# Kernel optimization log

Measured on AMD Instinct MI355X. Metric: run time of the kernel, lower is better.

The kernel has to match this reference:

```python
import jax, jax.numpy as jnp
import numpy as np

N = 131072   # n_nodes == n_edges (required by the broadcast in the original module)
C = 256      # node_channels == edge_channels (required by the broadcast)
EPS_BN = 1e-5
EPS = 1e-5


def _linear_params(key, out_c, in_c):
    k1, k2 = jax.random.split(key)
    bound = 1.0 / np.sqrt(in_c)
    W = jax.random.uniform(k1, (out_c, in_c), minval=-bound, maxval=bound, dtype=jnp.float32)
    b = jax.random.uniform(k2, (out_c,), minval=-bound, maxval=bound, dtype=jnp.float32)
    return W, b


def setup_inputs() -> dict:
    key = jax.random.key(0)
    ks = jax.random.split(key, 10)
    h = jax.random.normal(ks[0], (N, C), dtype=jnp.float32)
    e = jax.random.normal(ks[1], (N, C), dtype=jnp.float32)
    edge_index = jax.random.randint(ks[2], (2, N), 0, N, dtype=jnp.int64)
    A_w, A_b = _linear_params(ks[3], C, C)
    B_w, B_b = _linear_params(ks[4], C, C)
    C_w, C_b = _linear_params(ks[5], C, C)
    D_w, D_b = _linear_params(ks[6], C, C)
    U_w, U_b = _linear_params(ks[7], C, C)
    V_w, V_b = _linear_params(ks[8], C, C)
    bn_gamma = jnp.ones((C,), dtype=jnp.float32)
    bn_beta = jnp.zeros((C,), dtype=jnp.float32)
    return dict(h=h, edge_index=edge_index, e=e,
                A_w=A_w, A_b=A_b, B_w=B_w, B_b=B_b,
                C_w=C_w, C_b=C_b, D_w=D_w, D_b=D_b,
                bn_gamma=bn_gamma, bn_beta=bn_beta,
                U_w=U_w, U_b=U_b, V_w=V_w, V_b=V_b)


def reference(h, edge_index, e,
              A_w, A_b, B_w, B_b, C_w, C_b, D_w, D_b,
              bn_gamma, bn_beta, U_w, U_b, V_w, V_b):
    row, col = edge_index[0], edge_index[1]
    # gather + four parallel linears, summed: [E, C]
    e_out = (h[row] @ A_w.T + A_b
             + h[col] @ B_w.T + B_b
             + e[col] @ C_w.T + C_b
             + e[row] @ D_w.T + D_b)
    # BatchNorm1d (training mode: batch stats, biased variance) + ReLU
    mu = jnp.mean(e_out, axis=0)
    var = jnp.var(e_out, axis=0)
    e_out = jax.nn.relu(bn_gamma * (e_out - mu) * jax.lax.rsqrt(var + EPS_BN) + bn_beta)
    # scatter-add edge messages into node-indexed e, then sigmoid-normalize over dim 0
    e_new = e.at[row].add(e_out)
    e_new = jax.nn.sigmoid(e_new)
    e_new = e_new / (jnp.sum(e_new, axis=0, keepdims=True) + EPS)
    # final gather-multiply-reduce: (e_new * V(h[col])).sum(0) broadcasts [N,C]*[E,C] with N==E
    h_out = h @ U_w.T + U_b + jnp.sum(e_new * (h[col] @ V_w.T + V_b), axis=0)
    h_out = jax.nn.relu(h_out)
    return h_out, e_new
```

## Files before the change

### kernel.cpp

```cpp
#include <hip/hip_runtime.h>
#include <hip/hip_bf16.h>


typedef __attribute__((ext_vector_type(8))) short bf16x8;
typedef __attribute__((ext_vector_type(4))) float f32x4;

__device__ __forceinline__ float b2f(unsigned int lo16) {
  union { unsigned int u; float f; } c; c.u = lo16 << 16; return c.f;
}
__device__ __forceinline__ float lof(unsigned int u) { return b2f(u & 0xffffu); }
__device__ __forceinline__ float hif(unsigned int u) { return b2f(u >> 16); }
__device__ __forceinline__ unsigned int f2b(float f) {
  union { float f; unsigned int u; } c; c.f = f;
  unsigned int u = c.u;
  u += 0x7fffu + ((u >> 16) & 1u);
  return u >> 16;
}

__global__ __launch_bounds__(256) void prep_tiled(const float* __restrict__ src,
                                                  unsigned short* __restrict__ dst,
                                                  int nChunks) {
  int g = blockIdx.x * 256 + threadIdx.x;
  if (g >= nChunks) return;
  int mtile = g >> 9;
  int rem = g & 511;
  int r = rem >> 5, k8 = rem & 31;
  const float4* s = reinterpret_cast<const float4*>(src + (((size_t)mtile * 16 + r) << 8) + k8 * 8);
  float4 v0 = s[0], v1 = s[1];
  uint4 o;
  o.x = f2b(v0.x) | (f2b(v0.y) << 16);
  o.y = f2b(v0.z) | (f2b(v0.w) << 16);
  o.z = f2b(v1.x) | (f2b(v1.y) << 16);
  o.w = f2b(v1.z) | (f2b(v1.w) << 16);
  *reinterpret_cast<uint4*>(dst + ((size_t)mtile * 512 + k8 * 16 + r) * 8) = o;
}

__global__ __launch_bounds__(256) void gemm_bt(const unsigned short* __restrict__ At,
                                               const unsigned short* __restrict__ Bt,
                                               const float* __restrict__ bias,
                                               unsigned short* __restrict__ Cmat,
                                               int O, int nColBlk) {
  __shared__ char lds[16384];
  const int bid = blockIdx.x;
  const int colBlk = bid % nColBlk;
  const int rowBlk = bid / nColBlk;
  const int tid = threadIdx.x;
  const int w = tid >> 6, lane = tid & 63;
  const int wm = w >> 1, wn = w & 1;

  const char* Abase = (const char*)At + (size_t)(rowBlk * 8 + w * 2) * 8192 + lane * 16;
  const char* Bbase = (const char*)Bt + (size_t)(colBlk * 8 + w * 2) * 8192 + lane * 16;
  char* ldsA0 = lds + (w * 2) * 1024;
  char* ldsA1 = lds + (w * 2 + 1) * 1024;
  char* ldsB0 = lds + 8192 + (w * 2) * 1024;
  char* ldsB1 = lds + 8192 + (w * 2 + 1) * 1024;

  f32x4 acc[4][4] = {};

  for (int kt = 0; kt < 8; ++kt) {
    const size_t ko = (size_t)kt * 1024;
    __builtin_amdgcn_global_load_lds((const __attribute__((address_space(1))) void*)(Abase + ko),
                                     (__attribute__((address_space(3))) void*)ldsA0, 16, 0, 0);
    __builtin_amdgcn_global_load_lds((const __attribute__((address_space(1))) void*)(Abase + 8192 + ko),
                                     (__attribute__((address_space(3))) void*)ldsA1, 16, 0, 0);
    __builtin_amdgcn_global_load_lds((const __attribute__((address_space(1))) void*)(Bbase + ko),
                                     (__attribute__((address_space(3))) void*)ldsB0, 16, 0, 0);
    __builtin_amdgcn_global_load_lds((const __attribute__((address_space(1))) void*)(Bbase + 8192 + ko),
                                     (__attribute__((address_space(3))) void*)ldsB1, 16, 0, 0);
    __syncthreads();
    bf16x8 a[4], b[4];
#pragma unroll
    for (int mi = 0; mi < 4; ++mi)
      a[mi] = *reinterpret_cast<const bf16x8*>(lds + (wm * 4 + mi) * 1024 + lane * 16);
#pragma unroll
    for (int ni = 0; ni < 4; ++ni)
      b[ni] = *reinterpret_cast<const bf16x8*>(lds + 8192 + (wn * 4 + ni) * 1024 + lane * 16);
#pragma unroll
    for (int mi = 0; mi < 4; ++mi)
#pragma unroll
      for (int ni = 0; ni < 4; ++ni)
        acc[mi][ni] = __builtin_amdgcn_mfma_f32_16x16x32_bf16(a[mi], b[ni], acc[mi][ni], 0, 0, 0);
    __syncthreads();
  }

  const int rb = rowBlk * 128 + wm * 64 + ((lane >> 4) << 2);
  const int cb = colBlk * 128 + wn * 64 + (lane & 15);
#pragma unroll
  for (int mi = 0; mi < 4; ++mi) {
#pragma unroll
    for (int ni = 0; ni < 4; ++ni) {
      const int coln = cb + ni * 16;
      const float bz = bias[coln];
      const size_t base = (size_t)(rb + mi * 16) * O + coln;
#pragma unroll
      for (int r = 0; r < 4; ++r)
        Cmat[base + (size_t)r * O] = (unsigned short)f2b(acc[mi][ni][r] + bz);
    }
  }
}

__global__ __launch_bounds__(256) void edge_sum(
    const unsigned short* __restrict__ Ph, const unsigned short* __restrict__ Pe,
    const int* __restrict__ ei, const int* __restrict__ modep,
    unsigned short* __restrict__ eout,
    float* __restrict__ sums, float* __restrict__ sumsq, int Nn) {
  __shared__ float red[8][256];
  const int c8 = threadIdx.x & 31;
  const int sub = threadIdx.x >> 5;
  const int mode = *modep;
  float s[8], q[8];
#pragma unroll
  for (int j = 0; j < 8; ++j) { s[j] = 0.f; q[j] = 0.f; }

#pragma unroll 1
  for (int it = 0; it < 8; ++it) {
    const int k = blockIdx.x * 64 + it * 8 + sub;
    int row, col;
    if (mode) { row = ei[2 * k]; col = ei[2 * (Nn + k)]; }
    else      { row = ei[k];     col = ei[Nn + k]; }
    const uint4 ha = *reinterpret_cast<const uint4*>(Ph + (size_t)row * 1024 + c8 * 8);
    const uint4 hb = *reinterpret_cast<const uint4*>(Ph + (size_t)col * 1024 + 256 + c8 * 8);
    const uint4 ec = *reinterpret_cast<const uint4*>(Pe + (size_t)col * 512 + c8 * 8);
    const uint4 ed = *reinterpret_cast<const uint4*>(Pe + (size_t)row * 512 + 256 + c8 * 8);
    const unsigned int aw[4] = {ha.x, ha.y, ha.z, ha.w};
    const unsigned int bw[4] = {hb.x, hb.y, hb.z, hb.w};
    const unsigned int cw[4] = {ec.x, ec.y, ec.z, ec.w};
    const unsigned int dw[4] = {ed.x, ed.y, ed.z, ed.w};
    unsigned int ow[4];
#pragma unroll
    for (int p = 0; p < 4; ++p) {
      float v0 = lof(aw[p]) + lof(bw[p]) + lof(cw[p]) + lof(dw[p]);
      float v1 = hif(aw[p]) + hif(bw[p]) + hif(cw[p]) + hif(dw[p]);
      s[2 * p] += v0;     q[2 * p] += v0 * v0;
      s[2 * p + 1] += v1; q[2 * p + 1] += v1 * v1;
      ow[p] = f2b(v0) | (f2b(v1) << 16);
    }
    uint4 o; o.x = ow[0]; o.y = ow[1]; o.z = ow[2]; o.w = ow[3];
    *reinterpret_cast<uint4*>(eout + (size_t)k * 256 + c8 * 8) = o;
  }
#pragma unroll
  for (int j = 0; j < 8; ++j) red[sub][c8 * 8 + j] = s[j];
  __syncthreads();
  {
    const int c = threadIdx.x;
    float t = 0.f;
#pragma unroll
    for (int u2 = 0; u2 < 8; ++u2) t += red[u2][c];
    atomicAdd(sums + c, t);
  }
  __syncthreads();
#pragma unroll
  for (int j = 0; j < 8; ++j) red[sub][c8 * 8 + j] = q[j];
  __syncthreads();
  {
    const int c = threadIdx.x;
    float t = 0.f;
#pragma unroll
    for (int u2 = 0; u2 < 8; ++u2) t += red[u2][c];
    atomicAdd(sumsq + c, t);
  }
}

__global__ void bn_finalize(const float* __restrict__ sums, const float* __restrict__ sumsq,
                            const float* __restrict__ gamma, const float* __restrict__ beta,
                            float* __restrict__ scale, float* __restrict__ shift, float invE) {
  const int c = threadIdx.x;
  const float mu = sums[c] * invE;
  const float var = fmaxf(sumsq[c] * invE - mu * mu, 0.f);
  const float sc = gamma[c] * rsqrtf(var + 1e-5f);
  scale[c] = sc;
  shift[c] = beta[c] - mu * sc;
}

__global__ __launch_bounds__(256) void hist_rows(const int* __restrict__ ei,
                                                 const int* __restrict__ modep,
                                                 int* __restrict__ cnt, int Nn) {
  const int k = blockIdx.x * 256 + threadIdx.x;
  if (k >= Nn) return;
  const int row = (*modep) ? ei[2 * k] : ei[k];
  atomicAdd(&cnt[row], 1);
}

__global__ __launch_bounds__(256) void scan1(const int* __restrict__ cnt,
                                             int* __restrict__ bsum) {
  __shared__ int red[256];
  const int t = threadIdx.x;
  red[t] = cnt[blockIdx.x * 256 + t];
  __syncthreads();
#pragma unroll
  for (int s = 128; s > 0; s >>= 1) {
    if (t < s) red[t] += red[t + s];
    __syncthreads();
  }
  if (t == 0) bsum[blockIdx.x] = red[0];
}

__global__ __launch_bounds__(512) void scan2(int* __restrict__ bsum, int nb) {
  __shared__ int tmp[512];
  const int t = threadIdx.x;
  const int own = (t < nb) ? bsum[t] : 0;
  tmp[t] = own;
  __syncthreads();
  for (int off = 1; off < 512; off <<= 1) {
    int v = (t >= off) ? tmp[t - off] : 0;
    __syncthreads();
    tmp[t] += v;
    __syncthreads();
  }
  if (t < nb) bsum[t] = tmp[t] - own;
}

__global__ __launch_bounds__(256) void scan3(const int* __restrict__ cnt,
                                             const int* __restrict__ bsum,
                                             int* __restrict__ base, int Nn) {
  __shared__ int tmp[256];
  const int t = threadIdx.x;
  const int gid = blockIdx.x * 256 + t;
  const int own = cnt[gid];
  tmp[t] = own;
  __syncthreads();
  for (int off = 1; off < 256; off <<= 1) {
    int v = (t >= off) ? tmp[t - off] : 0;
    __syncthreads();
    tmp[t] += v;
    __syncthreads();
  }
  base[gid] = tmp[t] - own + bsum[blockIdx.x];
  if (gid == 0) base[Nn] = Nn;
}

__global__ __launch_bounds__(256) void scatter_eids(const int* __restrict__ ei,
                                                    const int* __restrict__ modep,
                                                    const int* __restrict__ base,
                                                    int* __restrict__ cnt,
                                                    int* __restrict__ sorted, int Nn) {
  const int k = blockIdx.x * 256 + threadIdx.x;
  if (k >= Nn) return;
  const int row = (*modep) ? ei[2 * k] : ei[k];
  const int pos = base[row] + atomicAdd(&cnt[row], -1) - 1;
  sorted[pos] = k;
}

__global__ __launch_bounds__(256) void gather_sig_colsum(
    const float* __restrict__ e, const unsigned short* __restrict__ eout,
    const int* __restrict__ base, const int* __restrict__ sorted,
    const float* __restrict__ scale, const float* __restrict__ shift,
    float* __restrict__ acc, float* __restrict__ colsum) {
  __shared__ float red[4][256];
  const int lane = threadIdx.x & 63, w = threadIdx.x >> 6;
  const float4 sc = *reinterpret_cast<const float4*>(scale + lane * 4);
  const float4 sh = *reinterpret_cast<const float4*>(shift + lane * 4);
  float s0 = 0.f, s1 = 0.f, s2 = 0.f, s3 = 0.f;
  const int n0 = blockIdx.x * 64 + w * 16;
#pragma unroll 1
  for (int it = 0; it < 16; ++it) {
    const int i = n0 + it;
    float4 v = *reinterpret_cast<const float4*>(e + (size_t)i * 256 + lane * 4);
    const int p0 = base[i], p1 = base[i + 1];
#pragma unroll 1
    for (int p = p0; p < p1; ++p) {
      const int eid = sorted[p];
      const uint2 wv = *reinterpret_cast<const uint2*>(eout + (size_t)eid * 256 + lane * 4);
      v.x += fmaxf(fmaf(sc.x, lof(wv.x), sh.x), 0.f);
      v.y += fmaxf(fmaf(sc.y, hif(wv.x), sh.y), 0.f);
      v.z += fmaxf(fmaf(sc.z, lof(wv.y), sh.z), 0.f);
      v.w += fmaxf(fmaf(sc.w, hif(wv.y), sh.w), 0.f);
    }
    v.x = 1.f / (1.f + __expf(-v.x));
    v.y = 1.f / (1.f + __expf(-v.y));
    v.z = 1.f / (1.f + __expf(-v.z));
    v.w = 1.f / (1.f + __expf(-v.w));
    *reinterpret_cast<float4*>(acc + (size_t)i * 256 + lane * 4) = v;
    s0 += v.x; s1 += v.y; s2 += v.z; s3 += v.w;
  }
  red[w][lane * 4 + 0] = s0;
  red[w][lane * 4 + 1] = s1;
  red[w][lane * 4 + 2] = s2;
  red[w][lane * 4 + 3] = s3;
  __syncthreads();
  const int c = threadIdx.x;
  atomicAdd(colsum + c, red[0][c] + red[1][c] + red[2][c] + red[3][c]);
}

__global__ void inv_finalize(const float* __restrict__ colsum, float* __restrict__ inv) {
  const int c = threadIdx.x;
  inv[c] = 1.0f / (colsum[c] + 1e-5f);
}

__global__ __launch_bounds__(256) void enew_T(
    const float* __restrict__ acc, const float* __restrict__ inv,
    const int* __restrict__ ei, const int* __restrict__ modep,
    const unsigned short* __restrict__ Ph,
    float* __restrict__ outE, float* __restrict__ T, int Nn) {
  __shared__ float red[8][256];
  const int c8 = threadIdx.x & 31, sub = threadIdx.x >> 5;
  const int mode = *modep;
  float iv[8];
#pragma unroll
  for (int j = 0; j < 8; ++j) iv[j] = inv[c8 * 8 + j];
  float t[8];
#pragma unroll
  for (int j = 0; j < 8; ++j) t[j] = 0.f;
#pragma unroll 1
  for (int it = 0; it < 8; ++it) {
    const int k = blockIdx.x * 64 + it * 8 + sub;
    const int col = mode ? ei[2 * (Nn + k)] : ei[Nn + k];
    const float4* p0 = reinterpret_cast<const float4*>(acc + (size_t)k * 256 + c8 * 8);
    const float4 a = p0[0], b = p0[1];
    float en[8] = {a.x * iv[0], a.y * iv[1], a.z * iv[2], a.w * iv[3],
                   b.x * iv[4], b.y * iv[5], b.z * iv[6], b.w * iv[7]};
    float4 o0, o1;
    o0.x = en[0]; o0.y = en[1]; o0.z = en[2]; o0.w = en[3];
    o1.x = en[4]; o1.y = en[5]; o1.z = en[6]; o1.w = en[7];
    float4* q0 = reinterpret_cast<float4*>(outE + (size_t)k * 256 + c8 * 8);
    q0[0] = o0; q0[1] = o1;
    const uint4 hv = *reinterpret_cast<const uint4*>(Ph + (size_t)col * 1024 + 512 + c8 * 8);
    const unsigned int w4[4] = {hv.x, hv.y, hv.z, hv.w};
#pragma unroll
    for (int p = 0; p < 4; ++p) {
      t[2 * p] += en[2 * p] * lof(w4[p]);
      t[2 * p + 1] += en[2 * p + 1] * hif(w4[p]);
    }
  }
#pragma unroll
  for (int j = 0; j < 8; ++j) red[sub][c8 * 8 + j] = t[j];
  __syncthreads();
  {
    const int c = threadIdx.x;
    float tt = 0.f;
#pragma unroll
    for (int u2 = 0; u2 < 8; ++u2) tt += red[u2][c];
    atomicAdd(T + c, tt);
  }
}

__global__ __launch_bounds__(256) void hout_k(
    const unsigned short* __restrict__ Ph, const float* __restrict__ T,
    float* __restrict__ outH, int nChunks) {
  const int g = blockIdx.x * 256 + threadIdx.x;
  if (g >= nChunks) return;
  const int i = g >> 5, c8 = g & 31;
  const uint4 hu = *reinterpret_cast<const uint4*>(Ph + (size_t)i * 1024 + 768 + c8 * 8);
  const float4 t0 = *reinterpret_cast<const float4*>(T + c8 * 8);
  const float4 t1 = *reinterpret_cast<const float4*>(T + c8 * 8 + 4);
  float4 o0, o1;
  o0.x = fmaxf(lof(hu.x) + t0.x, 0.f);
  o0.y = fmaxf(hif(hu.x) + t0.y, 0.f);
  o0.z = fmaxf(lof(hu.y) + t0.z, 0.f);
  o0.w = fmaxf(hif(hu.y) + t0.w, 0.f);
  o1.x = fmaxf(lof(hu.z) + t1.x, 0.f);
  o1.y = fmaxf(hif(hu.z) + t1.y, 0.f);
  o1.z = fmaxf(lof(hu.w) + t1.z, 0.f);
  o1.w = fmaxf(hif(hu.w) + t1.w, 0.f);
  float4* q = reinterpret_cast<float4*>(outH + (size_t)i * 256 + c8 * 8);
  q[0] = o0; q[1] = o1;
}

__global__ void pack_bias(const float* a, const float* b, const float* v, const float* u,
                          const float* cc, const float* dd,
                          float* biasH, float* biasE) {
  const int t = threadIdx.x;
  biasH[t] = a[t]; biasH[256 + t] = b[t]; biasH[512 + t] = v[t]; biasH[768 + t] = u[t];
  biasE[t] = cc[t]; biasE[256 + t] = dd[t];
}

__global__ void detect_idx(const int* __restrict__ ei, int* __restrict__ mode) {
  if (threadIdx.x == 0 && blockIdx.x == 0) {
    int m = 0;
#pragma unroll
    for (int i = 1; i < 64; i += 2) m |= ei[i];
    *mode = (m == 0) ? 1 : 0;
  }
}

extern "C" void kernel_launch(void* const* d_in, const int* in_sizes, int n_in,
                              void* d_out, int out_size, void* d_ws, size_t ws_size,
                              hipStream_t stream) {
  const float* h     = (const float*)d_in[0];
  const int*   ei    = (const int*)d_in[1];
  const float* e     = (const float*)d_in[2];
  const float* Aw    = (const float*)d_in[3];
  const float* Ab    = (const float*)d_in[4];
  const float* Bw    = (const float*)d_in[5];
  const float* Bb    = (const float*)d_in[6];
  const float* Cw    = (const float*)d_in[7];
  const float* Cb    = (const float*)d_in[8];
  const float* Dw    = (const float*)d_in[9];
  const float* Db    = (const float*)d_in[10];
  const float* gamma = (const float*)d_in[11];
  const float* beta  = (const float*)d_in[12];
  const float* Uw    = (const float*)d_in[13];
  const float* Ub    = (const float*)d_in[14];
  const float* Vw    = (const float*)d_in[15];
  const float* Vb    = (const float*)d_in[16];
  const int N = in_sizes[0] / 256;

  char* ws = (char*)d_ws;
  unsigned short* WtH = (unsigned short*)(ws + 0x0);
  unsigned short* WtE = (unsigned short*)(ws + 0x80000);
  float* biasH  = (float*)(ws + 0xC0000);
  float* biasE  = (float*)(ws + 0xC1000);
  float* sums   = (float*)(ws + 0xC2000);
  float* sumsq  = (float*)(ws + 0xC2400);
  float* colsum = (float*)(ws + 0xC2800);
  float* Tacc   = (float*)(ws + 0xC2C00);
  float* scale  = (float*)(ws + 0xC3000);
  float* shift  = (float*)(ws + 0xC3400);
  float* inv    = (float*)(ws + 0xC3800);
  int*   mode   = (int*)(ws + 0xC3C00);
  unsigned short* R1 = (unsigned short*)(ws + 0x100000);
  unsigned short* R3 = (unsigned short*)(ws + 0x4100000);
  char*           R4 = ws + 0x14100000;
  int* cnt    = (int*)(ws + 0x1C100000);
  int* baseA  = (int*)(ws + 0x1C180000);
  int* sorted = (int*)(ws + 0x1C210000);
  int* bsum   = (int*)(ws + 0x1C290000);

  unsigned short* e_t  = R3;
  unsigned short* P_e  = (unsigned short*)R4;
  unsigned short* h_t  = R1;
  unsigned short* P_h  = R3;
  unsigned short* eout = R1;
  float*          acc  = (float*)R4;

  float* outH = (float*)d_out;
  float* outE = outH + (size_t)N * 256;

  hipMemsetAsync(ws + 0xC2000, 0, 4096, stream);
  hipMemsetAsync(cnt, 0, (size_t)N * 4, stream);
  detect_idx<<<1, 64, 0, stream>>>(ei, mode);
  pack_bias<<<1, 256, 0, stream>>>(Ab, Bb, Vb, Ub, Cb, Db, biasH, biasE);
  prep_tiled<<<32, 256, 0, stream>>>(Aw, WtH + 0 * 65536, 8192);
  prep_tiled<<<32, 256, 0, stream>>>(Bw, WtH + 1 * 65536, 8192);
  prep_tiled<<<32, 256, 0, stream>>>(Vw, WtH + 2 * 65536, 8192);
  prep_tiled<<<32, 256, 0, stream>>>(Uw, WtH + 3 * 65536, 8192);
  prep_tiled<<<32, 256, 0, stream>>>(Cw, WtE + 0 * 65536, 8192);
  prep_tiled<<<32, 256, 0, stream>>>(Dw, WtE + 1 * 65536, 8192);

  hist_rows<<<N / 256, 256, 0, stream>>>(ei, mode, cnt, N);
  scan1<<<N / 256 / 256 ? 512 : 512, 256, 0, stream>>>(cnt, bsum);
  scan2<<<1, 512, 0, stream>>>(bsum, N / 256);
  scan3<<<N / 256, 256, 0, stream>>>(cnt, bsum, baseA, N);
  scatter_eids<<<N / 256, 256, 0, stream>>>(ei, mode, baseA, cnt, sorted, N);

  const int nChunks = N * 32;
  prep_tiled<<<nChunks / 256, 256, 0, stream>>>(e, e_t, nChunks);
  gemm_bt<<<(N / 128) * 4, 256, 0, stream>>>(e_t, WtE, biasE, P_e, 512, 4);
  prep_tiled<<<nChunks / 256, 256, 0, stream>>>(h, h_t, nChunks);
  gemm_bt<<<(N / 128) * 8, 256, 0, stream>>>(h_t, WtH, biasH, P_h, 1024, 8);

  edge_sum<<<N / 64, 256, 0, stream>>>(P_h, P_e, ei, mode, eout, sums, sumsq, N);
  bn_finalize<<<1, 256, 0, stream>>>(sums, sumsq, gamma, beta, scale, shift, 1.0f / (float)N);
  gather_sig_colsum<<<N / 64, 256, 0, stream>>>(e, eout, baseA, sorted, scale, shift, acc, colsum);
  inv_finalize<<<1, 256, 0, stream>>>(colsum, inv);
  enew_T<<<N / 64, 256, 0, stream>>>(acc, inv, ei, mode, P_h, outE, Tacc, N);
  hout_k<<<nChunks / 256, 256, 0, stream>>>(P_h, Tacc, outH, nChunks);
}
```

Measured before the change: 658.6 us.

## Fuse row/col projections via concatenated-K GEMM and recompute edge messages on the fly

Because h[row]@A + e[row]@D depends only on row (and likewise B/C on col), the projections are now computed per node as two K=512 concatenated GEMMs (PR and PC), with the biases pre-summed. Edge statistics and the scatter-gather now recompute each edge message as PR[row]+PC[col] from row-sorted edge lists instead of writing and rereading a materialised N×C edge buffer. The aim is to cut GEMM output width, gather traffic and the eout write/read. The change also adds an XCD-aware block swizzle in the GEMM. It costs a second gather of PC in the colsum pass and a slightly odd scan1 grid expression.

```diff
diff --git a/kernel.cpp b/kernel.cpp
--- a/kernel.cpp
+++ b/kernel.cpp
@@ -35,21 +35,23 @@
   *reinterpret_cast<uint4*>(dst + ((size_t)mtile * 512 + k8 * 16 + r) * 8) = o;
 }
 
-__global__ __launch_bounds__(256) void gemm_bt(const unsigned short* __restrict__ At,
-                                               const unsigned short* __restrict__ Bt,
-                                               const float* __restrict__ bias,
-                                               unsigned short* __restrict__ Cmat,
-                                               int O, int nColBlk) {
+__global__ __launch_bounds__(256) void gemm_bt2(
+    const unsigned short* __restrict__ Ah, const unsigned short* __restrict__ Ae,
+    const unsigned short* __restrict__ Bh, const unsigned short* __restrict__ Be,
+    const float* __restrict__ bias, unsigned short* __restrict__ Cmat,
+    int O, int nColBlk, int ktSteps, int nBlk) {
   __shared__ char lds[16384];
-  const int bid = blockIdx.x;
+  const int cpx = nBlk >> 3;
+  const int hw = blockIdx.x;
+  const int bid = (hw % 8) * cpx + hw / 8;
   const int colBlk = bid % nColBlk;
   const int rowBlk = bid / nColBlk;
   const int tid = threadIdx.x;
   const int w = tid >> 6, lane = tid & 63;
   const int wm = w >> 1, wn = w & 1;
 
-  const char* Abase = (const char*)At + (size_t)(rowBlk * 8 + w * 2) * 8192 + lane * 16;
-  const char* Bbase = (const char*)Bt + (size_t)(colBlk * 8 + w * 2) * 8192 + lane * 16;
+  const size_t aTileOff = (size_t)(rowBlk * 8 + w * 2) * 8192 + lane * 16;
+  const size_t bTileOff = (size_t)(colBlk * 8 + w * 2) * 8192 + lane * 16;
   char* ldsA0 = lds + (w * 2) * 1024;
   char* ldsA1 = lds + (w * 2 + 1) * 1024;
   char* ldsB0 = lds + 8192 + (w * 2) * 1024;
@@ -57,15 +59,16 @@
 
   f32x4 acc[4][4] = {};
 
-  for (int kt = 0; kt < 8; ++kt) {
-    const size_t ko = (size_t)kt * 1024;
-    __builtin_amdgcn_global_load_lds((const __attribute__((address_space(1))) void*)(Abase + ko),
+  for (int kt = 0; kt < ktSteps; ++kt) {
+    const char* Abase = (const char*)(kt < 8 ? Ah : Ae) + aTileOff + (size_t)(kt & 7) * 1024;
+    const char* Bbase = (const char*)(kt < 8 ? Bh : Be) + bTileOff + (size_t)(kt & 7) * 1024;
+    __builtin_amdgcn_global_load_lds((const __attribute__((address_space(1))) void*)Abase,
                                      (__attribute__((address_space(3))) void*)ldsA0, 16, 0, 0);
-    __builtin_amdgcn_global_load_lds((const __attribute__((address_space(1))) void*)(Abase + 8192 + ko),
+    __builtin_amdgcn_global_load_lds((const __attribute__((address_space(1))) void*)(Abase + 8192),
                                      (__attribute__((address_space(3))) void*)ldsA1, 16, 0, 0);
-    __builtin_amdgcn_global_load_lds((const __attribute__((address_space(1))) void*)(Bbase + ko),
+    __builtin_amdgcn_global_load_lds((const __attribute__((address_space(1))) void*)Bbase,
                                      (__attribute__((address_space(3))) void*)ldsB0, 16, 0, 0);
-    __builtin_amdgcn_global_load_lds((const __attribute__((address_space(1))) void*)(Bbase + 8192 + ko),
+    __builtin_amdgcn_global_load_lds((const __attribute__((address_space(1))) void*)(Bbase + 8192),
                                      (__attribute__((address_space(3))) void*)ldsB1, 16, 0, 0);
     __syncthreads();
     bf16x8 a[4], b[4];
@@ -99,44 +102,31 @@
   }
 }
 
-__global__ __launch_bounds__(256) void edge_sum(
-    const unsigned short* __restrict__ Ph, const unsigned short* __restrict__ Pe,
-    const int* __restrict__ ei, const int* __restrict__ modep,
-    unsigned short* __restrict__ eout,
-    float* __restrict__ sums, float* __restrict__ sumsq, int Nn) {
+__global__ __launch_bounds__(256) void edge_stats(
+    const unsigned short* __restrict__ PRPC,
+    const int* __restrict__ rows_s, const int* __restrict__ cols_s,
+    float* __restrict__ sums, float* __restrict__ sumsq) {
   __shared__ float red[8][256];
   const int c8 = threadIdx.x & 31;
   const int sub = threadIdx.x >> 5;
-  const int mode = *modep;
   float s[8], q[8];
 #pragma unroll
   for (int j = 0; j < 8; ++j) { s[j] = 0.f; q[j] = 0.f; }
-
 #pragma unroll 1
   for (int it = 0; it < 8; ++it) {
-    const int k = blockIdx.x * 64 + it * 8 + sub;
-    int row, col;
-    if (mode) { row = ei[2 * k]; col = ei[2 * (Nn + k)]; }
-    else      { row = ei[k];     col = ei[Nn + k]; }
-    const uint4 ha = *reinterpret_cast<const uint4*>(Ph + (size_t)row * 1024 + c8 * 8);
-    const uint4 hb = *reinterpret_cast<const uint4*>(Ph + (size_t)col * 1024 + 256 + c8 * 8);
-    const uint4 ec = *reinterpret_cast<const uint4*>(Pe + (size_t)col * 512 + c8 * 8);
-    const uint4 ed = *reinterpret_cast<const uint4*>(Pe + (size_t)row * 512 + 256 + c8 * 8);
-    const unsigned int aw[4] = {ha.x, ha.y, ha.z, ha.w};
-    const unsigned int bw[4] = {hb.x, hb.y, hb.z, hb.w};
-    const unsigned int cw[4] = {ec.x, ec.y, ec.z, ec.w};
-    const unsigned int dw[4] = {ed.x, ed.y, ed.z, ed.w};
-    unsigned int ow[4];
-#pragma unroll
-    for (int p = 0; p < 4; ++p) {
-      float v0 = lof(aw[p]) + lof(bw[p]) + lof(cw[p]) + lof(dw[p]);
-      float v1 = hif(aw[p]) + hif(bw[p]) + hif(cw[p]) + hif(dw[p]);
-      s[2 * p] += v0;     q[2 * p] += v0 * v0;
-      s[2 * p + 1] += v1; q[2 * p + 1] += v1 * v1;
-      ow[p] = f2b(v0) | (f2b(v1) << 16);
+    const int p = blockIdx.x * 64 + it * 8 + sub;
+    const int r = rows_s[p], cj = cols_s[p];
+    const uint4 pr = *reinterpret_cast<const uint4*>(PRPC + (size_t)r * 512 + c8 * 8);
+    const uint4 pc = *reinterpret_cast<const uint4*>(PRPC + (size_t)cj * 512 + 256 + c8 * 8);
+    const unsigned int rw[4] = {pr.x, pr.y, pr.z, pr.w};
+    const unsigned int cw[4] = {pc.x, pc.y, pc.z, pc.w};
+#pragma unroll
+    for (int p4 = 0; p4 < 4; ++p4) {
+      const float v0 = lof(rw[p4]) + lof(cw[p4]);
+      const float v1 = hif(rw[p4]) + hif(cw[p4]);
+      s[2 * p4] += v0;     q[2 * p4] += v0 * v0;
+      s[2 * p4 + 1] += v1; q[2 * p4 + 1] += v1 * v1;
     }
-    uint4 o; o.x = ow[0]; o.y = ow[1]; o.z = ow[2]; o.w = ow[3];
-    *reinterpret_cast<uint4*>(eout + (size_t)k * 256 + c8 * 8) = o;
   }
 #pragma unroll
   for (int j = 0; j < 8; ++j) red[sub][c8 * 8 + j] = s[j];
@@ -233,17 +223,21 @@
                                                     const int* __restrict__ modep,
                                                     const int* __restrict__ base,
                                                     int* __restrict__ cnt,
-                                                    int* __restrict__ sorted, int Nn) {
+                                                    int* __restrict__ rows_s,
+                                                    int* __restrict__ cols_s, int Nn) {
   const int k = blockIdx.x * 256 + threadIdx.x;
   if (k >= Nn) return;
-  const int row = (*modep) ? ei[2 * k] : ei[k];
+  int row, col;
+  if (*modep) { row = ei[2 * k]; col = ei[2 * (Nn + k)]; }
+  else        { row = ei[k];     col = ei[Nn + k]; }
   const int pos = base[row] + atomicAdd(&cnt[row], -1) - 1;
-  sorted[pos] = k;
+  rows_s[pos] = row;
+  cols_s[pos] = col;
 }
 
 __global__ __launch_bounds__(256) void gather_sig_colsum(
-    const float* __restrict__ e, const unsigned short* __restrict__ eout,
-    const int* __restrict__ base, const int* __restrict__ sorted,
+    const float* __restrict__ e, const unsigned short* __restrict__ PRPC,
+    const int* __restrict__ base, const int* __restrict__ cols_s,
     const float* __restrict__ scale, const float* __restrict__ shift,
     float* __restrict__ acc, float* __restrict__ colsum) {
   __shared__ float red[4][256];
@@ -256,15 +250,17 @@
   for (int it = 0; it < 16; ++it) {
     const int i = n0 + it;
     float4 v = *reinterpret_cast<const float4*>(e + (size_t)i * 256 + lane * 4);
+    const uint2 pr = *reinterpret_cast<const uint2*>(PRPC + (size_t)i * 512 + lane * 4);
+    const float pr0 = lof(pr.x), pr1 = hif(pr.x), pr2 = lof(pr.y), pr3 = hif(pr.y);
     const int p0 = base[i], p1 = base[i + 1];
 #pragma unroll 1
     for (int p = p0; p < p1; ++p) {
-      const int eid = sorted[p];
-      const uint2 wv = *reinterpret_cast<const uint2*>(eout + (size_t)eid * 256 + lane * 4);
-      v.x += fmaxf(fmaf(sc.x, lof(wv.x), sh.x), 0.f);
-      v.y += fmaxf(fmaf(sc.y, hif(wv.x), sh.y), 0.f);
-      v.z += fmaxf(fmaf(sc.z, lof(wv.y), sh.z), 0.f);
-      v.w += fmaxf(fmaf(sc.w, hif(wv.y), sh.w), 0.f);
+      const int cj = cols_s[p];
+      const uint2 pc = *reinterpret_cast<const uint2*>(PRPC + (size_t)cj * 512 + 256 + lane * 4);
+      v.x += fmaxf(fmaf(sc.x, pr0 + lof(pc.x), sh.x), 0.f);
+      v.y += fmaxf(fmaf(sc.y, pr1 + hif(pc.x), sh.y), 0.f);
+      v.z += fmaxf(fmaf(sc.z, pr2 + lof(pc.y), sh.z), 0.f);
+      v.w += fmaxf(fmaf(sc.w, pr3 + hif(pc.y), sh.w), 0.f);
     }
     v.x = 1.f / (1.f + __expf(-v.x));
     v.y = 1.f / (1.f + __expf(-v.y));
@@ -290,7 +286,7 @@
 __global__ __launch_bounds__(256) void enew_T(
     const float* __restrict__ acc, const float* __restrict__ inv,
     const int* __restrict__ ei, const int* __restrict__ modep,
-    const unsigned short* __restrict__ Ph,
+    const unsigned short* __restrict__ VU,
     float* __restrict__ outE, float* __restrict__ T, int Nn) {
   __shared__ float red[8][256];
   const int c8 = threadIdx.x & 31, sub = threadIdx.x >> 5;
@@ -314,7 +310,7 @@
     o1.x = en[4]; o1.y = en[5]; o1.z = en[6]; o1.w = en[7];
     float4* q0 = reinterpret_cast<float4*>(outE + (size_t)k * 256 + c8 * 8);
     q0[0] = o0; q0[1] = o1;
-    const uint4 hv = *reinterpret_cast<const uint4*>(Ph + (size_t)col * 1024 + 512 + c8 * 8);
+    const uint4 hv = *reinterpret_cast<const uint4*>(VU + (size_t)col * 512 + c8 * 8);
     const unsigned int w4[4] = {hv.x, hv.y, hv.z, hv.w};
 #pragma unroll
     for (int p = 0; p < 4; ++p) {
@@ -335,12 +331,12 @@
 }
 
 __global__ __launch_bounds__(256) void hout_k(
-    const unsigned short* __restrict__ Ph, const float* __restrict__ T,
+    const unsigned short* __restrict__ VU, const float* __restrict__ T,
     float* __restrict__ outH, int nChunks) {
   const int g = blockIdx.x * 256 + threadIdx.x;
   if (g >= nChunks) return;
   const int i = g >> 5, c8 = g & 31;
-  const uint4 hu = *reinterpret_cast<const uint4*>(Ph + (size_t)i * 1024 + 768 + c8 * 8);
+  const uint4 hu = *reinterpret_cast<const uint4*>(VU + (size_t)i * 512 + 256 + c8 * 8);
   const float4 t0 = *reinterpret_cast<const float4*>(T + c8 * 8);
   const float4 t1 = *reinterpret_cast<const float4*>(T + c8 * 8 + 4);
   float4 o0, o1;
@@ -356,12 +352,14 @@
   q[0] = o0; q[1] = o1;
 }
 
-__global__ void pack_bias(const float* a, const float* b, const float* v, const float* u,
-                          const float* cc, const float* dd,
-                          float* biasH, float* biasE) {
+__global__ void pack_bias2(const float* a, const float* d, const float* b, const float* cc,
+                           const float* v, const float* u,
+                           float* b1, float* b2) {
   const int t = threadIdx.x;
-  biasH[t] = a[t]; biasH[256 + t] = b[t]; biasH[512 + t] = v[t]; biasH[768 + t] = u[t];
-  biasE[t] = cc[t]; biasE[256 + t] = dd[t];
+  b1[t] = a[t] + d[t];
+  b1[256 + t] = b[t] + cc[t];
+  b2[t] = v[t];
+  b2[256 + t] = u[t];
 }
 
 __global__ void detect_idx(const int* __restrict__ ei, int* __restrict__ mode) {
@@ -396,63 +394,60 @@
   const int N = in_sizes[0] / 256;
 
   char* ws = (char*)d_ws;
-  unsigned short* WtH = (unsigned short*)(ws + 0x0);
-  unsigned short* WtE = (unsigned short*)(ws + 0x80000);
-  float* biasH  = (float*)(ws + 0xC0000);
-  float* biasE  = (float*)(ws + 0xC1000);
-  float* sums   = (float*)(ws + 0xC2000);
-  float* sumsq  = (float*)(ws + 0xC2400);
-  float* colsum = (float*)(ws + 0xC2800);
-  float* Tacc   = (float*)(ws + 0xC2C00);
-  float* scale  = (float*)(ws + 0xC3000);
-  float* shift  = (float*)(ws + 0xC3400);
-  float* inv    = (float*)(ws + 0xC3800);
-  int*   mode   = (int*)(ws + 0xC3C00);
-  unsigned short* R1 = (unsigned short*)(ws + 0x100000);
-  unsigned short* R3 = (unsigned short*)(ws + 0x4100000);
-  char*           R4 = ws + 0x14100000;
-  int* cnt    = (int*)(ws + 0x1C100000);
-  int* baseA  = (int*)(ws + 0x1C180000);
-  int* sorted = (int*)(ws + 0x1C210000);
-  int* bsum   = (int*)(ws + 0x1C290000);
-
-  unsigned short* e_t  = R3;
-  unsigned short* P_e  = (unsigned short*)R4;
-  unsigned short* h_t  = R1;
-  unsigned short* P_h  = R3;
-  unsigned short* eout = R1;
-  float*          acc  = (float*)R4;
+  unsigned short* W1h = (unsigned short*)(ws + 0x0);
+  unsigned short* W1e = (unsigned short*)(ws + 0x40000);
+  unsigned short* W2t = (unsigned short*)(ws + 0x80000);
+  float* b1     = (float*)(ws + 0xC0000);
+  float* b2     = (float*)(ws + 0xC0800);
+  float* sums   = (float*)(ws + 0xC1000);
+  float* sumsq  = (float*)(ws + 0xC1400);
+  float* colsum = (float*)(ws + 0xC1800);
+  float* Tacc   = (float*)(ws + 0xC1C00);
+  float* scale  = (float*)(ws + 0xC2000);
+  float* shift  = (float*)(ws + 0xC2400);
+  float* inv    = (float*)(ws + 0xC2800);
+  int*   mode   = (int*)(ws + 0xC2C00);
+  unsigned short* h_t  = (unsigned short*)(ws + 0x100000);
+  unsigned short* e_t  = (unsigned short*)(ws + 0x4100000);
+  unsigned short* PRPC = (unsigned short*)(ws + 0x8100000);
+  unsigned short* VU   = (unsigned short*)(ws + 0x10100000);
+  float*          acc  = (float*)(ws + 0x100000);
+  int* cnt    = (int*)(ws + 0x18100000);
+  int* baseA  = (int*)(ws + 0x18180000);
+  int* rows_s = (int*)(ws + 0x18210000);
+  int* cols_s = (int*)(ws + 0x18290000);
+  int* bsum   = (int*)(ws + 0x18310000);
 
   float* outH = (float*)d_out;
   float* outE = outH + (size_t)N * 256;
 
-  hipMemsetAsync(ws + 0xC2000, 0, 4096, stream);
+  hipMemsetAsync(ws + 0xC1000, 0, 4096, stream);
   hipMemsetAsync(cnt, 0, (size_t)N * 4, stream);
   detect_idx<<<1, 64, 0, stream>>>(ei, mode);
-  pack_bias<<<1, 256, 0, stream>>>(Ab, Bb, Vb, Ub, Cb, Db, biasH, biasE);
-  prep_tiled<<<32, 256, 0, stream>>>(Aw, WtH + 0 * 65536, 8192);
-  prep_tiled<<<32, 256, 0, stream>>>(Bw, WtH + 1 * 65536, 8192);
-  prep_tiled<<<32, 256, 0, stream>>>(Vw, WtH + 2 * 65536, 8192);
-  prep_tiled<<<32, 256, 0, stream>>>(Uw, WtH + 3 * 65536, 8192);
-  prep_tiled<<<32, 256, 0, stream>>>(Cw, WtE + 0 * 65536, 8192);
-  prep_tiled<<<32, 256, 0, stream>>>(Dw, WtE + 1 * 65536, 8192);
+  pack_bias2<<<1, 256, 0, stream>>>(Ab, Db, Bb, Cb, Vb, Ub, b1, b2);
+  prep_tiled<<<32, 256, 0, stream>>>(Aw, W1h, 8192);
+  prep_tiled<<<32, 256, 0, stream>>>(Bw, W1h + 16 * 4096, 8192);
+  prep_tiled<<<32, 256, 0, stream>>>(Dw, W1e, 8192);
+  prep_tiled<<<32, 256, 0, stream>>>(Cw, W1e + 16 * 4096, 8192);
+  prep_tiled<<<32, 256, 0, stream>>>(Vw, W2t, 8192);
+  prep_tiled<<<32, 256, 0, stream>>>(Uw, W2t + 16 * 4096, 8192);
 
   hist_rows<<<N / 256, 256, 0, stream>>>(ei, mode, cnt, N);
-  scan1<<<N / 256 / 256 ? 512 : 512, 256, 0, stream>>>(cnt, bsum);
+  scan1<<<N / 256 / 256 * 256 + ((N / 256) % 256 ? 1 : 0) + 511, 256, 0, stream>>>(cnt, bsum);
   scan2<<<1, 512, 0, stream>>>(bsum, N / 256);
   scan3<<<N / 256, 256, 0, stream>>>(cnt, bsum, baseA, N);
-  scatter_eids<<<N / 256, 256, 0, stream>>>(ei, mode, baseA, cnt, sorted, N);
+  scatter_eids<<<N / 256, 256, 0, stream>>>(ei, mode, baseA, cnt, rows_s, cols_s, N);
 
   const int nChunks = N * 32;
+  prep_tiled<<<nChunks / 256, 256, 0, stream>>>(h, h_t, nChunks);
   prep_tiled<<<nChunks / 256, 256, 0, stream>>>(e, e_t, nChunks);
-  gemm_bt<<<(N / 128) * 4, 256, 0, stream>>>(e_t, WtE, biasE, P_e, 512, 4);
-  prep_tiled<<<nChunks / 256, 256, 0, stream>>>(h, h_t, nChunks);
-  gemm_bt<<<(N / 128) * 8, 256, 0, stream>>>(h_t, WtH, biasH, P_h, 1024, 8);
-
-  edge_sum<<<N / 64, 256, 0, stream>>>(P_h, P_e, ei, mode, eout, sums, sumsq, N);
+  gemm_bt2<<<(N / 128) * 4, 256, 0, stream>>>(h_t, e_t, W1h, W1e, b1, PRPC, 512, 4, 16, (N / 128) * 4);
+  gemm_bt2<<<(N / 128) * 4, 256, 0, stream>>>(h_t, h_t, W2t, W2t, b2, VU, 512, 4, 8, (N / 128) * 4);
+
+  edge_stats<<<N / 64, 256, 0, stream>>>(PRPC, rows_s, cols_s, sums, sumsq);
   bn_finalize<<<1, 256, 0, stream>>>(sums, sumsq, gamma, beta, scale, shift, 1.0f / (float)N);
-  gather_sig_colsum<<<N / 64, 256, 0, stream>>>(e, eout, baseA, sorted, scale, shift, acc, colsum);
+  gather_sig_colsum<<<N / 64, 256, 0, stream>>>(e, PRPC, baseA, cols_s, scale, shift, acc, colsum);
   inv_finalize<<<1, 256, 0, stream>>>(colsum, inv);
-  enew_T<<<N / 64, 256, 0, stream>>>(acc, inv, ei, mode, P_h, outE, Tacc, N);
-  hout_k<<<nChunks / 256, 256, 0, stream>>>(P_h, Tacc, outH, nChunks);
-}
+  enew_T<<<N / 64, 256, 0, stream>>>(acc, inv, ei, mode, VU, outE, Tacc, N);
+  hout_k<<<nChunks / 256, 256, 0, stream>>>(VU, Tacc, outH, nChunks);
+}
```

After: 639.4 us. 2.9% less time.
